# Performance work log

Hardware: AMD Instinct MI355X
Metric: run time of the kernel (lower is better)

Reference implementation:

```python
import jax, jax.numpy as jnp
import numpy as np

N = 50000        # nodes
E = 640000       # edges
D = 128          # emb_dim
L = 3            # num_layer
EDGE_DIM = 8
BN_EPS = 1e-5


def setup_inputs() -> dict:
    key = jax.random.key(0)
    ks = jax.random.split(key, 6)
    return dict(
        x=jax.random.normal(ks[0], (N, D), jnp.float32),
        edge_index=jax.random.randint(ks[1], (2, E), 0, N),
        edge_attr=jax.random.normal(ks[2], (E, EDGE_DIM), jnp.float32),
        eps=jnp.zeros((L,), jnp.float32),
        We=jax.random.normal(ks[3], (L, EDGE_DIM, D), jnp.float32) * 0.1,
        be=jnp.zeros((L, D), jnp.float32),
        W1=jax.random.normal(ks[4], (L, D, 2 * D), jnp.float32) * (1.0 / np.sqrt(D)),
        b1=jnp.zeros((L, 2 * D), jnp.float32),
        g1=jnp.ones((L, 2 * D), jnp.float32),
        bt1=jnp.zeros((L, 2 * D), jnp.float32),
        W2=jax.random.normal(ks[5], (L, 2 * D, D), jnp.float32) * (1.0 / np.sqrt(2 * D)),
        b2=jnp.zeros((L, D), jnp.float32),
        gbn=jnp.ones((L, D), jnp.float32),
        bbn=jnp.zeros((L, D), jnp.float32),
    )


def _bn(h, g, b):
    # BatchNorm1d, training-mode statistics over the node/batch axis
    mu = h.mean(axis=0)
    var = h.var(axis=0)
    return (h - mu) * jax.lax.rsqrt(var + BN_EPS) * g + b


def reference(x, edge_index, edge_attr, eps, We, be, W1, b1, g1, bt1, W2, b2, gbn, bbn):
    src, dst = edge_index[0], edge_index[1]
    h = x
    for l in range(L):
        # GINConv: edge-encoded messages, relu, scatter-add aggregation
        ee = edge_attr @ We[l] + be[l]                      # [E, D]
        msg = jax.nn.relu(h[src] + ee)                      # [E, D]
        agg = jax.ops.segment_sum(msg, dst, num_segments=N)  # [N, D]
        z = (1.0 + eps[l]) * h + agg
        # GIN MLP: Linear -> BN -> ReLU -> Linear
        z = jax.nn.relu(_bn(z @ W1[l] + b1[l], g1[l], bt1[l]))
        z = z @ W2[l] + b2[l]
        # outer per-layer BatchNorm; ReLU on all but the last layer (dropout = eval identity)
        z = _bn(z, gbn[l], bbn[l])
        if l < L - 1:
            z = jax.nn.relu(z)
        h = z  # residual=False, so no skip add
    return h  # JK == 'last'
```

## Files before the change

### kernel.cpp

```cpp
#include <hip/hip_runtime.h>

#define N_NODES 50000
#define N_EDGES 640000
#define D 128
#define D2 256
#define BN_EPS 1e-5f

typedef unsigned short ushort_t;
typedef unsigned int uint_t;

using bf16x8 = __attribute__((ext_vector_type(8))) short;
using f32x4  = __attribute__((ext_vector_type(4))) float;

__device__ inline ushort_t f2bf(float f) {
    uint_t u = __builtin_bit_cast(uint_t, f);
    u = (u + 0x7fffu + ((u >> 16) & 1u)) >> 16;
    return (ushort_t)u;
}
__device__ inline float bf2f(uint_t bits_lo16) {
    return __builtin_bit_cast(float, bits_lo16 << 16);
}

__global__ __launch_bounds__(256) void hist_kernel(
    const int* __restrict__ dst, int* __restrict__ hist)
{
    const int e = blockIdx.x * 256 + threadIdx.x;
    if (e < N_EDGES) atomicAdd(&hist[dst[e]], 1);
}

__global__ __launch_bounds__(256) void scan1_kernel(
    const int* __restrict__ hist, int* __restrict__ scanA,
    int* __restrict__ bsum)
{
    __shared__ int sm[256];
    const int t = threadIdx.x;
    const int idx = blockIdx.x * 256 + t;
    int val = (idx < N_NODES) ? hist[idx] : 0;
    sm[t] = val;
    __syncthreads();
#pragma unroll
    for (int off = 1; off < 256; off <<= 1) {
        const int add = (t >= off) ? sm[t - off] : 0;
        __syncthreads();
        val += add;
        sm[t] = val;
        __syncthreads();
    }
    scanA[idx] = val;
    if (t == 255) bsum[blockIdx.x] = val;
}

__global__ __launch_bounds__(256) void scan2_kernel(
    const int* __restrict__ bsum, int* __restrict__ bscan, int nb)
{
    __shared__ int sm[256];
    const int t = threadIdx.x;
    int val = (t < nb) ? bsum[t] : 0;
    sm[t] = val;
    __syncthreads();
#pragma unroll
    for (int off = 1; off < 256; off <<= 1) {
        const int add = (t >= off) ? sm[t - off] : 0;
        __syncthreads();
        val += add;
        sm[t] = val;
        __syncthreads();
    }
    bscan[t] = val;
}

__global__ __launch_bounds__(256) void scan3_kernel(
    const int* __restrict__ hist, const int* __restrict__ scanA,
    const int* __restrict__ bscan, int* __restrict__ excl)
{
    const int idx = blockIdx.x * 256 + threadIdx.x;
    if (idx < N_NODES) {
        const int carry = blockIdx.x ? bscan[blockIdx.x - 1] : 0;
        const int incl = scanA[idx] + carry;
        excl[idx] = incl - hist[idx];
        if (idx == N_NODES - 1) excl[N_NODES] = incl;
    }
}

__global__ __launch_bounds__(256) void scatter_kernel(
    const int* __restrict__ src, const int* __restrict__ dst,
    const float* __restrict__ ea, int* __restrict__ cursor,
    int* __restrict__ srcp_s, float* __restrict__ ea_s)
{
    const int e = blockIdx.x * 256 + threadIdx.x;
    if (e < N_EDGES) {
        const int t = dst[e];
        const int p = atomicAdd(&cursor[t], 1);
        srcp_s[p] = src[e];
        *(float4*)&ea_s[(size_t)p * 8]     = *(const float4*)&ea[(size_t)e * 8];
        *(float4*)&ea_s[(size_t)p * 8 + 4] = *(const float4*)&ea[(size_t)e * 8 + 4];
    }
}

__global__ __launch_bounds__(256) void wtrans_kernel(
    const float* __restrict__ in, ushort_t* __restrict__ out, int K, int Nt)
{
    __shared__ float tile[32][33];
    const int l = blockIdx.z;
    in  += (size_t)l * K * Nt;
    out += (size_t)l * K * Nt;
    const int n0 = blockIdx.x * 32, k0 = blockIdx.y * 32;
    const int tx = threadIdx.x & 31, ty = threadIdx.x >> 5;
#pragma unroll
    for (int i = 0; i < 32; i += 8)
        tile[ty + i][tx] = in[(size_t)(k0 + ty + i) * Nt + n0 + tx];
    __syncthreads();
#pragma unroll
    for (int i = 0; i < 32; i += 8)
        out[(size_t)(n0 + ty + i) * K + k0 + tx] = f2bf(tile[tx][ty + i]);
}

__device__ __forceinline__ void msg_accum(
    const float* __restrict__ hv, const float* __restrict__ eav,
    const float (&wv)[8][8], const float* __restrict__ bev,
    float* __restrict__ acc)
{
    float m[8];
#pragma unroll
    for (int j = 0; j < 8; ++j) m[j] = bev[j];
#pragma unroll
    for (int k = 0; k < 8; ++k)
#pragma unroll
        for (int j = 0; j < 8; ++j)
            m[j] = fmaf(eav[k], wv[k][j], m[j]);
#pragma unroll
    for (int j = 0; j < 8; ++j)
        acc[j] += fmaxf(hv[j] + m[j], 0.f);
}

__device__ __forceinline__ void unpack_bn_relu(
    const uint4 v, const float* __restrict__ scv,
    const float* __restrict__ shv, float* __restrict__ hv)
{
    float f[8];
    f[0] = bf2f(v.x & 0xffffu); f[1] = bf2f(v.x >> 16);
    f[2] = bf2f(v.y & 0xffffu); f[3] = bf2f(v.y >> 16);
    f[4] = bf2f(v.z & 0xffffu); f[5] = bf2f(v.z >> 16);
    f[6] = bf2f(v.w & 0xffffu); f[7] = bf2f(v.w >> 16);
#pragma unroll
    for (int j = 0; j < 8; ++j)
        hv[j] = fmaxf(fmaf(f[j], scv[j], shv[j]), 0.f);
}

__device__ __forceinline__ void store_z(
    ushort_t* __restrict__ z, int node, int d0, float epsv,
    const float* __restrict__ hn, const float* __restrict__ acc)
{
    uint_t w[8];
#pragma unroll
    for (int j = 0; j < 8; ++j)
        w[j] = (uint_t)f2bf(fmaf(epsv, hn[j], acc[j]));
    uint4 o;
    o.x = w[0] | (w[1] << 16);
    o.y = w[2] | (w[3] << 16);
    o.z = w[4] | (w[5] << 16);
    o.w = w[6] | (w[7] << 16);
    *(uint4*)&z[(size_t)node * D + d0] = o;
}

__global__ __launch_bounds__(256) void agg_z_f32_kernel(
    const float* __restrict__ h, const int* __restrict__ excl,
    const int* __restrict__ srcp_s, const float* __restrict__ ea_s,
    const float* __restrict__ We_l, const float* __restrict__ be_l,
    const float* __restrict__ eps_l, ushort_t* __restrict__ z)
{
    const int lane = threadIdx.x & 63;
    const int wave = threadIdx.x >> 6;
    const int node = blockIdx.x * 4 + wave;
    const int grp  = lane >> 4;
    const int gl   = lane & 15;
    const int d0   = gl * 8;

    float wv[8][8];
#pragma unroll
    for (int k = 0; k < 8; ++k) {
        *(float4*)&wv[k][0] = *(const float4*)&We_l[k * D + d0];
        *(float4*)&wv[k][4] = *(const float4*)&We_l[k * D + d0 + 4];
    }
    float bev[8];
    *(float4*)&bev[0] = *(const float4*)&be_l[d0];
    *(float4*)&bev[4] = *(const float4*)&be_l[d0 + 4];

    const int p0 = excl[node];
    const int p1 = excl[node + 1];
    const int deg = p1 - p0;
    const int scached = (lane < deg) ? srcp_s[p0 + lane] : 0;
    const int nmain = deg < 64 ? deg : 64;

    float acc[8] = {0.f, 0.f, 0.f, 0.f, 0.f, 0.f, 0.f, 0.f};

    if (deg > 0) {
        const int niter = (nmain + 7) >> 3;
        int qA = grp, qB = grp + 4;
        float eA[8], hA[8], eB[8], hB[8];
        for (int it = 0; it < niter - 1; ++it) {
            const int sA = __shfl(scached, qA);
            const int sB = __shfl(scached, qB);
            *(float4*)&eA[0] = *(const float4*)&ea_s[(size_t)(p0 + qA) * 8];
            *(float4*)&eA[4] = *(const float4*)&ea_s[(size_t)(p0 + qA) * 8 + 4];
            *(float4*)&hA[0] = *(const float4*)&h[(size_t)sA * D + d0];
            *(float4*)&hA[4] = *(const float4*)&h[(size_t)sA * D + d0 + 4];
            *(float4*)&eB[0] = *(const float4*)&ea_s[(size_t)(p0 + qB) * 8];
            *(float4*)&eB[4] = *(const float4*)&ea_s[(size_t)(p0 + qB) * 8 + 4];
            *(float4*)&hB[0] = *(const float4*)&h[(size_t)sB * D + d0];
            *(float4*)&hB[4] = *(const float4*)&h[(size_t)sB * D + d0 + 4];
            msg_accum(hA, eA, wv, bev, acc);
            msg_accum(hB, eB, wv, bev, acc);
            qA += 8; qB += 8;
        }
        const int cA = (qA < nmain) ? qA : 0;
        const int cB = (qB < nmain) ? qB : 0;
        const int sA = __shfl(scached, cA);
        const int sB = __shfl(scached, cB);
        if (qA < nmain) {
            *(float4*)&eA[0] = *(const float4*)&ea_s[(size_t)(p0 + qA) * 8];
            *(float4*)&eA[4] = *(const float4*)&ea_s[(size_t)(p0 + qA) * 8 + 4];
            *(float4*)&hA[0] = *(const float4*)&h[(size_t)sA * D + d0];
            *(float4*)&hA[4] = *(const float4*)&h[(size_t)sA * D + d0 + 4];
            msg_accum(hA, eA, wv, bev, acc);
        }
        if (qB < nmain) {
            *(float4*)&eB[0] = *(const float4*)&ea_s[(size_t)(p0 + qB) * 8];
            *(float4*)&eB[4] = *(const float4*)&ea_s[(size_t)(p0 + qB) * 8 + 4];
            *(float4*)&hB[0] = *(const float4*)&h[(size_t)sB * D + d0];
            *(float4*)&hB[4] = *(const float4*)&h[(size_t)sB * D + d0 + 4];
            msg_accum(hB, eB, wv, bev, acc);
        }
    }
    for (int p = p0 + 64 + grp; p < p1; p += 4) {
        const int s = srcp_s[p];
        float eT[8], hT[8];
        *(float4*)&eT[0] = *(const float4*)&ea_s[(size_t)p * 8];
        *(float4*)&eT[4] = *(const float4*)&ea_s[(size_t)p * 8 + 4];
        *(float4*)&hT[0] = *(const float4*)&h[(size_t)s * D + d0];
        *(float4*)&hT[4] = *(const float4*)&h[(size_t)s * D + d0 + 4];
        msg_accum(hT, eT, wv, bev, acc);
    }

#pragma unroll
    for (int j = 0; j < 8; ++j) {
        acc[j] += __shfl_xor(acc[j], 16);
        acc[j] += __shfl_xor(acc[j], 32);
    }

    if (grp == 0) {
        float hn[8];
        *(float4*)&hn[0] = *(const float4*)&h[(size_t)node * D + d0];
        *(float4*)&hn[4] = *(const float4*)&h[(size_t)node * D + d0 + 4];
        store_z(z, node, d0, 1.0f + eps_l[0], hn, acc);
    }
}

__global__ __launch_bounds__(256) void agg_z_bf16_kernel(
    const ushort_t* __restrict__ t2, const float* __restrict__ sc2,
    const float* __restrict__ sh2, const int* __restrict__ excl,
    const int* __restrict__ srcp_s, const float* __restrict__ ea_s,
    const float* __restrict__ We_l, const float* __restrict__ be_l,
    const float* __restrict__ eps_l, ushort_t* __restrict__ z)
{
    const int lane = threadIdx.x & 63;
    const int wave = threadIdx.x >> 6;
    const int node = blockIdx.x * 4 + wave;
    const int grp  = lane >> 4;
    const int gl   = lane & 15;
    const int d0   = gl * 8;

    float wv[8][8];
#pragma unroll
    for (int k = 0; k < 8; ++k) {
        *(float4*)&wv[k][0] = *(const float4*)&We_l[k * D + d0];
        *(float4*)&wv[k][4] = *(const float4*)&We_l[k * D + d0 + 4];
    }
    float bev[8], scv[8], shv[8];
    *(float4*)&bev[0] = *(const float4*)&be_l[d0];
    *(float4*)&bev[4] = *(const float4*)&be_l[d0 + 4];
    *(float4*)&scv[0] = *(const float4*)&sc2[d0];
    *(float4*)&scv[4] = *(const float4*)&sc2[d0 + 4];
    *(float4*)&shv[0] = *(const float4*)&sh2[d0];
    *(float4*)&shv[4] = *(const float4*)&sh2[d0 + 4];

    const int p0 = excl[node];
    const int p1 = excl[node + 1];
    const int deg = p1 - p0;
    const int scached = (lane < deg) ? srcp_s[p0 + lane] : 0;
    const int nmain = deg < 64 ? deg : 64;

    float acc[8] = {0.f, 0.f, 0.f, 0.f, 0.f, 0.f, 0.f, 0.f};

    if (deg > 0) {
        const int niter = (nmain + 7) >> 3;
        int qA = grp, qB = grp + 4;
        float eA[8], eB[8], hA[8], hB[8];
        uint4 vA, vB;
        for (int it = 0; it < niter - 1; ++it) {
            const int sA = __shfl(scached, qA);
            const int sB = __shfl(scached, qB);
            *(float4*)&eA[0] = *(const float4*)&ea_s[(size_t)(p0 + qA) * 8];
            *(float4*)&eA[4] = *(const float4*)&ea_s[(size_t)(p0 + qA) * 8 + 4];
            vA = *(const uint4*)&t2[(size_t)sA * D + d0];
            *(float4*)&eB[0] = *(const float4*)&ea_s[(size_t)(p0 + qB) * 8];
            *(float4*)&eB[4] = *(const float4*)&ea_s[(size_t)(p0 + qB) * 8 + 4];
            vB = *(const uint4*)&t2[(size_t)sB * D + d0];
            unpack_bn_relu(vA, scv, shv, hA);
            msg_accum(hA, eA, wv, bev, acc);
            unpack_bn_relu(vB, scv, shv, hB);
            msg_accum(hB, eB, wv, bev, acc);
            qA += 8; qB += 8;
        }
        const int cA = (qA < nmain) ? qA : 0;
        const int cB = (qB < nmain) ? qB : 0;
        const int sA = __shfl(scached, cA);
        const int sB = __shfl(scached, cB);
        if (qA < nmain) {
            *(float4*)&eA[0] = *(const float4*)&ea_s[(size_t)(p0 + qA) * 8];
            *(float4*)&eA[4] = *(const float4*)&ea_s[(size_t)(p0 + qA) * 8 + 4];
            vA = *(const uint4*)&t2[(size_t)sA * D + d0];
            unpack_bn_relu(vA, scv, shv, hA);
            msg_accum(hA, eA, wv, bev, acc);
        }
        if (qB < nmain) {
            *(float4*)&eB[0] = *(const float4*)&ea_s[(size_t)(p0 + qB) * 8];
            *(float4*)&eB[4] = *(const float4*)&ea_s[(size_t)(p0 + qB) * 8 + 4];
            vB = *(const uint4*)&t2[(size_t)sB * D + d0];
            unpack_bn_relu(vB, scv, shv, hB);
            msg_accum(hB, eB, wv, bev, acc);
        }
    }
    for (int p = p0 + 64 + grp; p < p1; p += 4) {
        const int s = srcp_s[p];
        float eT[8], hT[8];
        *(float4*)&eT[0] = *(const float4*)&ea_s[(size_t)p * 8];
        *(float4*)&eT[4] = *(const float4*)&ea_s[(size_t)p * 8 + 4];
        const uint4 vT = *(const uint4*)&t2[(size_t)s * D + d0];
        unpack_bn_relu(vT, scv, shv, hT);
        msg_accum(hT, eT, wv, bev, acc);
    }

#pragma unroll
    for (int j = 0; j < 8; ++j) {
        acc[j] += __shfl_xor(acc[j], 16);
        acc[j] += __shfl_xor(acc[j], 32);
    }

    if (grp == 0) {
        const uint4 vN = *(const uint4*)&t2[(size_t)node * D + d0];
        float hn[8];
        unpack_bn_relu(vN, scv, shv, hn);
        store_z(z, node, d0, 1.0f + eps_l[0], hn, acc);
    }
}

template<int KTILES>
__global__ __launch_bounds__(256) void gemm_bf16_kernel(
    const ushort_t* __restrict__ A, const ushort_t* __restrict__ Bt,
    const float* __restrict__ bias, ushort_t* __restrict__ out,
    float* __restrict__ gsum, float* __restrict__ gsq)
{
    __shared__ ushort_t As[128][136];
    __shared__ ushort_t Bs[128][136];
    __shared__ float ls_sum[128], ls_sq[128];
    const int tid = threadIdx.x;
    const int M0 = blockIdx.x * 128;
    const int N0 = blockIdx.y * 128;
    const int Ntot = gridDim.y * 128;
    const int K = KTILES * 128;
    if (tid < 128) { ls_sum[tid] = 0.f; ls_sq[tid] = 0.f; }
    const int lane = tid & 63, w = tid >> 6;
    const int wm = w >> 1, wn = w & 1;
    const int lr = lane & 15;
    const int lk = (lane >> 4) * 8;
    f32x4 acc[4][4] = {};

    for (int kt = 0; kt < KTILES; ++kt) {
        if (kt) __syncthreads();
#pragma unroll
        for (int p = 0; p < 8; ++p) {
            const int idx = p * 256 + tid;
            const int row = idx >> 4, ch = (idx & 15) * 8;
            uint4 v = make_uint4(0, 0, 0, 0);
            const int gr = M0 + row;
            if (gr < N_NODES)
                v = *(const uint4*)&A[(size_t)gr * K + kt * 128 + ch];
            *(uint4*)&As[row][ch] = v;
        }
#pragma unroll
        for (int p = 0; p < 8; ++p) {
            const int idx = p * 256 + tid;
            const int row = idx >> 4, ch = (idx & 15) * 8;
            *(uint4*)&Bs[row][ch] =
                *(const uint4*)&Bt[(size_t)(N0 + row) * K + kt * 128 + ch];
        }
        __syncthreads();
#pragma unroll
        for (int ks = 0; ks < 4; ++ks) {
            const int kof = ks * 32 + lk;
            bf16x8 af[4], bfr[4];
#pragma unroll
            for (int mi = 0; mi < 4; ++mi)
                af[mi] = *(const bf16x8*)&As[wm * 64 + mi * 16 + lr][kof];
#pragma unroll
            for (int ni = 0; ni < 4; ++ni)
                bfr[ni] = *(const bf16x8*)&Bs[wn * 64 + ni * 16 + lr][kof];
#pragma unroll
            for (int mi = 0; mi < 4; ++mi)
#pragma unroll
                for (int ni = 0; ni < 4; ++ni)
                    acc[mi][ni] = __builtin_amdgcn_mfma_f32_16x16x32_bf16(
                        af[mi], bfr[ni], acc[mi][ni], 0, 0, 0);
        }
    }
    __syncthreads();

#pragma unroll
    for (int ni = 0; ni < 4; ++ni) {
        const int cl = wn * 64 + ni * 16 + lr;
        const float bv = bias[N0 + cl];
        float ps = 0.f, pq = 0.f;
#pragma unroll
        for (int mi = 0; mi < 4; ++mi) {
            const int rbase = M0 + wm * 64 + mi * 16 + (lane >> 4) * 4;
#pragma unroll
            for (int r = 0; r < 4; ++r) {
                const int row = rbase + r;
                if (row < N_NODES) {
                    const float v = acc[mi][ni][r] + bv;
                    out[(size_t)row * Ntot + N0 + cl] = f2bf(v);
                    ps += v;
                    pq += v * v;
                }
            }
        }
        atomicAdd(&ls_sum[cl], ps);
        atomicAdd(&ls_sq[cl], pq);
    }
    __syncthreads();
    if (tid < 128) {
        unsafeAtomicAdd(&gsum[N0 + tid], ls_sum[tid]);
        unsafeAtomicAdd(&gsq[N0 + tid], ls_sq[tid]);
    }
}

__global__ __launch_bounds__(256) void gemm2_bn_kernel(
    const ushort_t* __restrict__ A, const float* __restrict__ sc1,
    const float* __restrict__ sh1, const ushort_t* __restrict__ Bt,
    const float* __restrict__ bias, ushort_t* __restrict__ out,
    float* __restrict__ gsum, float* __restrict__ gsq)
{
    __shared__ ushort_t As[128][136];
    __shared__ ushort_t Bs[128][136];
    __shared__ float ls_sum[128], ls_sq[128];
    const int tid = threadIdx.x;
    const int M0 = blockIdx.x * 128;
    const int K = 256, Ntot = 128;
    if (tid < 128) { ls_sum[tid] = 0.f; ls_sq[tid] = 0.f; }
    const int lane = tid & 63, w = tid >> 6;
    const int wm = w >> 1, wn = w & 1;
    const int lr = lane & 15;
    const int lk = (lane >> 4) * 8;
    f32x4 acc[4][4] = {};

    for (int kt = 0; kt < 2; ++kt) {
        if (kt) __syncthreads();
#pragma unroll
        for (int p = 0; p < 8; ++p) {
            const int idx = p * 256 + tid;
            const int row = idx >> 4, ch = (idx & 15) * 8;
            const int col = kt * 128 + ch;
            uint4 v = make_uint4(0, 0, 0, 0);
            const int gr = M0 + row;
            if (gr < N_NODES) {
                const uint4 t = *(const uint4*)&A[(size_t)gr * K + col];
                float f[8];
                f[0] = bf2f(t.x & 0xffffu); f[1] = bf2f(t.x >> 16);
                f[2] = bf2f(t.y & 0xffffu); f[3] = bf2f(t.y >> 16);
                f[4] = bf2f(t.z & 0xffffu); f[5] = bf2f(t.z >> 16);
                f[6] = bf2f(t.w & 0xffffu); f[7] = bf2f(t.w >> 16);
                const float4 s0 = *(const float4*)&sc1[col];
                const float4 s1 = *(const float4*)&sc1[col + 4];
                const float4 h0 = *(const float4*)&sh1[col];
                const float4 h1 = *(const float4*)&sh1[col + 4];
                f[0] = fmaxf(fmaf(f[0], s0.x, h0.x), 0.f);
                f[1] = fmaxf(fmaf(f[1], s0.y, h0.y), 0.f);
                f[2] = fmaxf(fmaf(f[2], s0.z, h0.z), 0.f);
                f[3] = fmaxf(fmaf(f[3], s0.w, h0.w), 0.f);
                f[4] = fmaxf(fmaf(f[4], s1.x, h1.x), 0.f);
                f[5] = fmaxf(fmaf(f[5], s1.y, h1.y), 0.f);
                f[6] = fmaxf(fmaf(f[6], s1.z, h1.z), 0.f);
                f[7] = fmaxf(fmaf(f[7], s1.w, h1.w), 0.f);
                v.x = (uint_t)f2bf(f[0]) | ((uint_t)f2bf(f[1]) << 16);
                v.y = (uint_t)f2bf(f[2]) | ((uint_t)f2bf(f[3]) << 16);
                v.z = (uint_t)f2bf(f[4]) | ((uint_t)f2bf(f[5]) << 16);
                v.w = (uint_t)f2bf(f[6]) | ((uint_t)f2bf(f[7]) << 16);
            }
            *(uint4*)&As[row][ch] = v;
        }
#pragma unroll
        for (int p = 0; p < 8; ++p) {
            const int idx = p * 256 + tid;
            const int row = idx >> 4, ch = (idx & 15) * 8;
            *(uint4*)&Bs[row][ch] =
                *(const uint4*)&Bt[(size_t)row * K + kt * 128 + ch];
        }
        __syncthreads();
#pragma unroll
        for (int ks = 0; ks < 4; ++ks) {
            const int kof = ks * 32 + lk;
            bf16x8 af[4], bfr[4];
#pragma unroll
            for (int mi = 0; mi < 4; ++mi)
                af[mi] = *(const bf16x8*)&As[wm * 64 + mi * 16 + lr][kof];
#pragma unroll
            for (int ni = 0; ni < 4; ++ni)
                bfr[ni] = *(const bf16x8*)&Bs[wn * 64 + ni * 16 + lr][kof];
#pragma unroll
            for (int mi = 0; mi < 4; ++mi)
#pragma unroll
                for (int ni = 0; ni < 4; ++ni)
                    acc[mi][ni] = __builtin_amdgcn_mfma_f32_16x16x32_bf16(
                        af[mi], bfr[ni], acc[mi][ni], 0, 0, 0);
        }
    }
    __syncthreads();

#pragma unroll
    for (int ni = 0; ni < 4; ++ni) {
        const int cl = wn * 64 + ni * 16 + lr;
        const float bv = bias[cl];
        float ps = 0.f, pq = 0.f;
#pragma unroll
        for (int mi = 0; mi < 4; ++mi) {
            const int rbase = M0 + wm * 64 + mi * 16 + (lane >> 4) * 4;
#pragma unroll
            for (int r = 0; r < 4; ++r) {
                const int row = rbase + r;
                if (row < N_NODES) {
                    const float v = acc[mi][ni][r] + bv;
                    out[(size_t)row * Ntot + cl] = f2bf(v);
                    ps += v;
                    pq += v * v;
                }
            }
        }
        atomicAdd(&ls_sum[cl], ps);
        atomicAdd(&ls_sq[cl], pq);
    }
    __syncthreads();
    if (tid < 128) {
        unsafeAtomicAdd(&gsum[tid], ls_sum[tid]);
        unsafeAtomicAdd(&gsq[tid], ls_sq[tid]);
    }
}

__global__ void bnparam_kernel(const float* __restrict__ gsum,
                               const float* __restrict__ gsq,
                               const float* __restrict__ g,
                               const float* __restrict__ bt,
                               float* __restrict__ scale,
                               float* __restrict__ shift, int C)
{
    const int c = threadIdx.x;
    if (c < C) {
        const float inv_n = 1.0f / (float)N_NODES;
        const float mu = gsum[c] * inv_n;
        const float var = gsq[c] * inv_n - mu * mu;
        const float s = g[c] * rsqrtf(var + BN_EPS);
        scale[c] = s;
        shift[c] = bt[c] - mu * s;
    }
}

__global__ __launch_bounds__(256) void bnapply2_kernel(
    const ushort_t* __restrict__ t, const float* __restrict__ sc,
    const float* __restrict__ sh, float* __restrict__ outp)
{
    const size_t idx = (size_t)blockIdx.x * 256 + threadIdx.x;
    const int c = (int)(idx & 15) * 8;
    const uint4 v = ((const uint4*)t)[idx];
    const float4 s0 = *(const float4*)&sc[c];
    const float4 s1 = *(const float4*)&sc[c + 4];
    const float4 h0 = *(const float4*)&sh[c];
    const float4 h1 = *(const float4*)&sh[c + 4];
    float4 r0, r1;
    r0.x = fmaf(bf2f(v.x & 0xffffu), s0.x, h0.x);
    r0.y = fmaf(bf2f(v.x >> 16),     s0.y, h0.y);
    r0.z = fmaf(bf2f(v.y & 0xffffu), s0.z, h0.z);
    r0.w = fmaf(bf2f(v.y >> 16),     s0.w, h0.w);
    r1.x = fmaf(bf2f(v.z & 0xffffu), s1.x, h1.x);
    r1.y = fmaf(bf2f(v.z >> 16),     s1.y, h1.y);
    r1.z = fmaf(bf2f(v.w & 0xffffu), s1.z, h1.z);
    r1.w = fmaf(bf2f(v.w >> 16),     s1.w, h1.w);
    *(float4*)&outp[idx * 8]     = r0;
    *(float4*)&outp[idx * 8 + 4] = r1;
}

extern "C" void kernel_launch(void* const* d_in, const int* in_sizes, int n_in,
                              void* d_out, int out_size, void* d_ws, size_t ws_size,
                              hipStream_t stream)
{
    const float* x         = (const float*)d_in[0];
    const int*   edge_index= (const int*)d_in[1];
    const float* edge_attr = (const float*)d_in[2];
    const float* eps       = (const float*)d_in[3];
    const float* We        = (const float*)d_in[4];
    const float* be        = (const float*)d_in[5];
    const float* W1        = (const float*)d_in[6];
    const float* b1        = (const float*)d_in[7];
    const float* g1        = (const float*)d_in[8];
    const float* bt1       = (const float*)d_in[9];
    const float* W2        = (const float*)d_in[10];
    const float* b2        = (const float*)d_in[11];
    const float* gbn       = (const float*)d_in[12];
    const float* bbn       = (const float*)d_in[13];
    float* out = (float*)d_out;

    float* ws = (float*)d_ws;
    const size_t ND = (size_t)N_NODES * D;
    float* EAS  = ws;
    float* ZB   = EAS + (size_t)N_EDGES * 8;
    float* T2B  = ZB + ND / 2;
    float* T1B  = T2B + ND / 2;
    float* STATS = T1B + ND;
    float* gsum1 = STATS;
    float* gsq1  = gsum1 + 3 * 256;
    float* gsum2 = gsq1 + 3 * 256;
    float* gsq2  = gsum2 + 3 * 128;
    float* scale1 = gsq2 + 3 * 128;
    float* shift1 = scale1 + 256;
    float* sc2buf = shift1 + 256;
    float* sh2buf = sc2buf + 3 * 128;

    ushort_t* zbuf  = (ushort_t*)ZB;
    ushort_t* t2buf = (ushort_t*)T2B;
    ushort_t* t1buf = (ushort_t*)T1B;

    int* hist   = (int*)T1B;
    int* scanA  = hist + N_NODES;
    int* bsum   = scanA + 50176;
    int* bscan  = bsum + 256;
    int* cursor = bscan + 256;

    int* srcp_s = (int*)d_out;
    int* excl   = srcp_s + N_EDGES;
    ushort_t* W1t = (ushort_t*)((int*)d_out + 690008);
    ushort_t* W2t = W1t + 3 * D2 * D;

    const int* srcp = edge_index;
    const int* dstp = edge_index + N_EDGES;

    hipMemsetAsync(STATS, 0, 2304 * sizeof(float), stream);
    hipMemsetAsync(hist, 0, N_NODES * sizeof(int), stream);

    const int EB = (N_EDGES + 255) / 256;
    const int NB = (N_NODES + 255) / 256;
    hist_kernel<<<EB, 256, 0, stream>>>(dstp, hist);
    scan1_kernel<<<NB, 256, 0, stream>>>(hist, scanA, bsum);
    scan2_kernel<<<1, 256, 0, stream>>>(bsum, bscan, NB);
    scan3_kernel<<<NB, 256, 0, stream>>>(hist, scanA, bscan, excl);
    hipMemcpyAsync(cursor, excl, N_NODES * sizeof(int),
                   hipMemcpyDeviceToDevice, stream);
    scatter_kernel<<<EB, 256, 0, stream>>>(srcp, dstp, edge_attr,
                                           cursor, srcp_s, EAS);

    wtrans_kernel<<<dim3(8, 4, 3), 256, 0, stream>>>(W1, W1t, D, D2);
    wtrans_kernel<<<dim3(4, 8, 3), 256, 0, stream>>>(W2, W2t, D2, D);

    for (int l = 0; l < 3; ++l) {
        if (l == 0) {
            agg_z_f32_kernel<<<N_NODES / 4, 256, 0, stream>>>(
                x, excl, srcp_s, EAS,
                We + (size_t)l * 8 * D, be + (size_t)l * D, eps + l, zbuf);
        } else {
            agg_z_bf16_kernel<<<N_NODES / 4, 256, 0, stream>>>(
                t2buf, sc2buf + (l - 1) * 128, sh2buf + (l - 1) * 128,
                excl, srcp_s, EAS,
                We + (size_t)l * 8 * D, be + (size_t)l * D, eps + l, zbuf);
        }

        dim3 grid1((N_NODES + 127) / 128, 2);
        gemm_bf16_kernel<1><<<grid1, 256, 0, stream>>>(
            zbuf, W1t + (size_t)l * D2 * D, b1 + (size_t)l * D2,
            t1buf, gsum1 + l * 256, gsq1 + l * 256);

        bnparam_kernel<<<1, 256, 0, stream>>>(
            gsum1 + l * 256, gsq1 + l * 256,
            g1 + (size_t)l * D2, bt1 + (size_t)l * D2, scale1, shift1, D2);

        dim3 grid2((N_NODES + 127) / 128, 1);
        gemm2_bn_kernel<<<grid2, 256, 0, stream>>>(
            t1buf, scale1, shift1,
            W2t + (size_t)l * D * D2, b2 + (size_t)l * D, t2buf,
            gsum2 + l * 128, gsq2 + l * 128);

        bnparam_kernel<<<1, 256, 0, stream>>>(
            gsum2 + l * 128, gsq2 + l * 128,
            gbn + (size_t)l * D, bbn + (size_t)l * D,
            sc2buf + l * 128, sh2buf + l * 128, D);
    }

    bnapply2_kernel<<<(N_NODES * D / 8) / 256, 256, 0, stream>>>(
        t2buf, sc2buf + 2 * 128, sh2buf + 2 * 128, out);
}
```

Measured before the change: 656.5 us.

## Replace LDS-tiled GEMMs with register-resident weight fragments and direct global A loads

```diff
diff --git a/kernel.cpp b/kernel.cpp
--- a/kernel.cpp
+++ b/kernel.cpp
@@ -355,81 +355,62 @@
     }
 }
 
-template<int KTILES>
-__global__ __launch_bounds__(256) void gemm_bf16_kernel(
+__global__ __launch_bounds__(256) void gemm1_reg_kernel(
     const ushort_t* __restrict__ A, const ushort_t* __restrict__ Bt,
     const float* __restrict__ bias, ushort_t* __restrict__ out,
     float* __restrict__ gsum, float* __restrict__ gsq)
 {
-    __shared__ ushort_t As[128][136];
-    __shared__ ushort_t Bs[128][136];
-    __shared__ float ls_sum[128], ls_sq[128];
+    __shared__ float ls_sum[D2], ls_sq[D2];
     const int tid = threadIdx.x;
-    const int M0 = blockIdx.x * 128;
-    const int N0 = blockIdx.y * 128;
-    const int Ntot = gridDim.y * 128;
-    const int K = KTILES * 128;
-    if (tid < 128) { ls_sum[tid] = 0.f; ls_sq[tid] = 0.f; }
-    const int lane = tid & 63, w = tid >> 6;
-    const int wm = w >> 1, wn = w & 1;
+    const int lane = tid & 63, wn = tid >> 6;
     const int lr = lane & 15;
     const int lk = (lane >> 4) * 8;
+    const int M0 = blockIdx.x * 64;
+    ls_sum[tid] = 0.f; ls_sq[tid] = 0.f;
+    __syncthreads();
+
+    bf16x8 bfr[4][4];
+#pragma unroll
+    for (int ni = 0; ni < 4; ++ni)
+#pragma unroll
+        for (int ks = 0; ks < 4; ++ks)
+            bfr[ni][ks] = *(const bf16x8*)
+                &Bt[(size_t)(wn * 64 + ni * 16 + lr) * D + ks * 32 + lk];
+
+    const bf16x8 zfrag = {};
     f32x4 acc[4][4] = {};
-
-    for (int kt = 0; kt < KTILES; ++kt) {
-        if (kt) __syncthreads();
-#pragma unroll
-        for (int p = 0; p < 8; ++p) {
-            const int idx = p * 256 + tid;
-            const int row = idx >> 4, ch = (idx & 15) * 8;
-            uint4 v = make_uint4(0, 0, 0, 0);
-            const int gr = M0 + row;
-            if (gr < N_NODES)
-                v = *(const uint4*)&A[(size_t)gr * K + kt * 128 + ch];
-            *(uint4*)&As[row][ch] = v;
-        }
-#pragma unroll
-        for (int p = 0; p < 8; ++p) {
-            const int idx = p * 256 + tid;
-            const int row = idx >> 4, ch = (idx & 15) * 8;
-            *(uint4*)&Bs[row][ch] =
-                *(const uint4*)&Bt[(size_t)(N0 + row) * K + kt * 128 + ch];
-        }
-        __syncthreads();
-#pragma unroll
-        for (int ks = 0; ks < 4; ++ks) {
-            const int kof = ks * 32 + lk;
-            bf16x8 af[4], bfr[4];
-#pragma unroll
-            for (int mi = 0; mi < 4; ++mi)
-                af[mi] = *(const bf16x8*)&As[wm * 64 + mi * 16 + lr][kof];
+#pragma unroll
+    for (int ks = 0; ks < 4; ++ks) {
+        bf16x8 af[4];
+#pragma unroll
+        for (int mi = 0; mi < 4; ++mi) {
+            const int row = M0 + mi * 16 + lr;
+            af[mi] = (row < N_NODES)
+                ? *(const bf16x8*)&A[(size_t)row * D + ks * 32 + lk]
+                : zfrag;
+        }
+#pragma unroll
+        for (int mi = 0; mi < 4; ++mi)
 #pragma unroll
             for (int ni = 0; ni < 4; ++ni)
-                bfr[ni] = *(const bf16x8*)&Bs[wn * 64 + ni * 16 + lr][kof];
-#pragma unroll
-            for (int mi = 0; mi < 4; ++mi)
-#pragma unroll
-                for (int ni = 0; ni < 4; ++ni)
-                    acc[mi][ni] = __builtin_amdgcn_mfma_f32_16x16x32_bf16(
-                        af[mi], bfr[ni], acc[mi][ni], 0, 0, 0);
-        }
-    }
-    __syncthreads();
+                acc[mi][ni] = __builtin_amdgcn_mfma_f32_16x16x32_bf16(
+                    af[mi], bfr[ni][ks], acc[mi][ni], 0, 0, 0);
+    }
 
 #pragma unroll
     for (int ni = 0; ni < 4; ++ni) {
         const int cl = wn * 64 + ni * 16 + lr;
-        const float bv = bias[N0 + cl];
+        const float bv = bias[cl];
         float ps = 0.f, pq = 0.f;
 #pragma unroll
         for (int mi = 0; mi < 4; ++mi) {
-            const int rbase = M0 + wm * 64 + mi * 16 + (lane >> 4) * 4;
+            const int rbase = M0 + mi * 16 + (lane >> 4) * 4;
 #pragma unroll
             for (int r = 0; r < 4; ++r) {
                 const int row = rbase + r;
                 if (row < N_NODES) {
                     const float v = acc[mi][ni][r] + bv;
-                    out[(size_t)row * Ntot + N0 + cl] = f2bf(v);
+                    out[(size_t)row * D2 + cl] = f2bf(v);
                     ps += v;
                     pq += v * v;
                 }
@@ -439,108 +420,86 @@
         atomicAdd(&ls_sq[cl], pq);
     }
     __syncthreads();
-    if (tid < 128) {
-        unsafeAtomicAdd(&gsum[N0 + tid], ls_sum[tid]);
-        unsafeAtomicAdd(&gsq[N0 + tid], ls_sq[tid]);
-    }
-}
-
-__global__ __launch_bounds__(256) void gemm2_bn_kernel(
+    unsafeAtomicAdd(&gsum[tid], ls_sum[tid]);
+    unsafeAtomicAdd(&gsq[tid], ls_sq[tid]);
+}
+
+__global__ __launch_bounds__(256) void gemm2_reg_kernel(
     const ushort_t* __restrict__ A, const float* __restrict__ sc1,
     const float* __restrict__ sh1, const ushort_t* __restrict__ Bt,
     const float* __restrict__ bias, ushort_t* __restrict__ out,
     float* __restrict__ gsum, float* __restrict__ gsq)
 {
-    __shared__ ushort_t As[128][136];
-    __shared__ ushort_t Bs[128][136];
-    __shared__ float ls_sum[128], ls_sq[128];
+    __shared__ float ls_sum[D], ls_sq[D];
     const int tid = threadIdx.x;
-    const int M0 = blockIdx.x * 128;
-    const int K = 256, Ntot = 128;
-    if (tid < 128) { ls_sum[tid] = 0.f; ls_sq[tid] = 0.f; }
-    const int lane = tid & 63, w = tid >> 6;
-    const int wm = w >> 1, wn = w & 1;
+    const int lane = tid & 63, wn = tid >> 6;
     const int lr = lane & 15;
     const int lk = (lane >> 4) * 8;
-    f32x4 acc[4][4] = {};
-
-    for (int kt = 0; kt < 2; ++kt) {
-        if (kt) __syncthreads();
-#pragma unroll
-        for (int p = 0; p < 8; ++p) {
-            const int idx = p * 256 + tid;
-            const int row = idx >> 4, ch = (idx & 15) * 8;
-            const int col = kt * 128 + ch;
-            uint4 v = make_uint4(0, 0, 0, 0);
-            const int gr = M0 + row;
-            if (gr < N_NODES) {
-                const uint4 t = *(const uint4*)&A[(size_t)gr * K + col];
+    const int M0 = blockIdx.x * 64;
+    if (tid < D) { ls_sum[tid] = 0.f; ls_sq[tid] = 0.f; }
+    __syncthreads();
+
+    bf16x8 bfr[2][8];
+#pragma unroll
+    for (int ni = 0; ni < 2; ++ni)
+#pragma unroll
+        for (int ks = 0; ks < 8; ++ks)
+            bfr[ni][ks] = *(const bf16x8*)
+                &Bt[(size_t)(wn * 32 + ni * 16 + lr) * D2 + ks * 32 + lk];
+
+    f32x4 acc[4][2] = {};
+#pragma unroll
+    for (int ks = 0; ks < 8; ++ks) {
+        const int kc = ks * 32 + lk;
+        float scv[8], shv[8];
+        *(float4*)&scv[0] = *(const float4*)&sc1[kc];
+        *(float4*)&scv[4] = *(const float4*)&sc1[kc + 4];
+        *(float4*)&shv[0] = *(const float4*)&sh1[kc];
+        *(float4*)&shv[4] = *(const float4*)&sh1[kc + 4];
+        bf16x8 af[4];
+#pragma unroll
+        for (int mi = 0; mi < 4; ++mi) {
+            const int row = M0 + mi * 16 + lr;
+            uint4 pk = make_uint4(0, 0, 0, 0);
+            if (row < N_NODES) {
+                const uint4 t = *(const uint4*)&A[(size_t)row * D2 + kc];
                 float f[8];
                 f[0] = bf2f(t.x & 0xffffu); f[1] = bf2f(t.x >> 16);
                 f[2] = bf2f(t.y & 0xffffu); f[3] = bf2f(t.y >> 16);
                 f[4] = bf2f(t.z & 0xffffu); f[5] = bf2f(t.z >> 16);
                 f[6] = bf2f(t.w & 0xffffu); f[7] = bf2f(t.w >> 16);
-                const float4 s0 = *(const float4*)&sc1[col];
-                const float4 s1 = *(const float4*)&sc1[col + 4];
-                const float4 h0 = *(const float4*)&sh1[col];
-                const float4 h1 = *(const float4*)&sh1[col + 4];
-                f[0] = fmaxf(fmaf(f[0], s0.x, h0.x), 0.f);
-                f[1] = fmaxf(fmaf(f[1], s0.y, h0.y), 0.f);
-                f[2] = fmaxf(fmaf(f[2], s0.z, h0.z), 0.f);
-                f[3] = fmaxf(fmaf(f[3], s0.w, h0.w), 0.f);
-                f[4] = fmaxf(fmaf(f[4], s1.x, h1.x), 0.f);
-                f[5] = fmaxf(fmaf(f[5], s1.y, h1.y), 0.f);
-                f[6] = fmaxf(fmaf(f[6], s1.z, h1.z), 0.f);
-                f[7] = fmaxf(fmaf(f[7], s1.w, h1.w), 0.f);
-                v.x = (uint_t)f2bf(f[0]) | ((uint_t)f2bf(f[1]) << 16);
-                v.y = (uint_t)f2bf(f[2]) | ((uint_t)f2bf(f[3]) << 16);
-                v.z = (uint_t)f2bf(f[4]) | ((uint_t)f2bf(f[5]) << 16);
-                v.w = (uint_t)f2bf(f[6]) | ((uint_t)f2bf(f[7]) << 16);
+#pragma unroll
+                for (int j = 0; j < 8; ++j)
+                    f[j] = fmaxf(fmaf(f[j], scv[j], shv[j]), 0.f);
+                pk.x = (uint_t)f2bf(f[0]) | ((uint_t)f2bf(f[1]) << 16);
+                pk.y = (uint_t)f2bf(f[2]) | ((uint_t)f2bf(f[3]) << 16);
+                pk.z = (uint_t)f2bf(f[4]) | ((uint_t)f2bf(f[5]) << 16);
+                pk.w = (uint_t)f2bf(f[6]) | ((uint_t)f2bf(f[7]) << 16);
             }
-            *(uint4*)&As[row][ch] = v;
-        }
-#pragma unroll
-        for (int p = 0; p < 8; ++p) {
-            const int idx = p * 256 + tid;
-            const int row = idx >> 4, ch = (idx & 15) * 8;
-            *(uint4*)&Bs[row][ch] =
-                *(const uint4*)&Bt[(size_t)row * K + kt * 128 + ch];
-        }
-        __syncthreads();
-#pragma unroll
-        for (int ks = 0; ks < 4; ++ks) {
-            const int kof = ks * 32 + lk;
-            bf16x8 af[4], bfr[4];
-#pragma unroll
-            for (int mi = 0; mi < 4; ++mi)
-                af[mi] = *(const bf16x8*)&As[wm * 64 + mi * 16 + lr][kof];
-#pragma unroll
-            for (int ni = 0; ni < 4; ++ni)
-                bfr[ni] = *(const bf16x8*)&Bs[wn * 64 + ni * 16 + lr][kof];
-#pragma unroll
-            for (int mi = 0; mi < 4; ++mi)
-#pragma unroll
-                for (int ni = 0; ni < 4; ++ni)
-                    acc[mi][ni] = __builtin_amdgcn_mfma_f32_16x16x32_bf16(
-                        af[mi], bfr[ni], acc[mi][ni], 0, 0, 0);
-        }
-    }
-    __syncthreads();
-
-#pragma unroll
-    for (int ni = 0; ni < 4; ++ni) {
-        const int cl = wn * 64 + ni * 16 + lr;
+            af[mi] = __builtin_bit_cast(bf16x8, pk);
+        }
+#pragma unroll
+        for (int mi = 0; mi < 4; ++mi)
+#pragma unroll
+            for (int ni = 0; ni < 2; ++ni)
+                acc[mi][ni] = __builtin_amdgcn_mfma_f32_16x16x32_bf16(
+                    af[mi], bfr[ni][ks], acc[mi][ni], 0, 0, 0);
+    }
+
+#pragma unroll
+    for (int ni = 0; ni < 2; ++ni) {
+        const int cl = wn * 32 + ni * 16 + lr;
         const float bv = bias[cl];
         float ps = 0.f, pq = 0.f;
 #pragma unroll
         for (int mi = 0; mi < 4; ++mi) {
-            const int rbase = M0 + wm * 64 + mi * 16 + (lane >> 4) * 4;
+            const int rbase = M0 + mi * 16 + (lane >> 4) * 4;
 #pragma unroll
             for (int r = 0; r < 4; ++r) {
                 const int row = rbase + r;
                 if (row < N_NODES) {
                     const float v = acc[mi][ni][r] + bv;
-                    out[(size_t)row * Ntot + cl] = f2bf(v);
+                    out[(size_t)row * D + cl] = f2bf(v);
                     ps += v;
                     pq += v * v;
                 }
@@ -550,7 +509,7 @@
         atomicAdd(&ls_sq[cl], pq);
     }
     __syncthreads();
-    if (tid < 128) {
+    if (tid < D) {
         unsafeAtomicAdd(&gsum[tid], ls_sum[tid]);
         unsafeAtomicAdd(&gsq[tid], ls_sq[tid]);
     }
@@ -669,6 +628,8 @@
     wtrans_kernel<<<dim3(8, 4, 3), 256, 0, stream>>>(W1, W1t, D, D2);
     wtrans_kernel<<<dim3(4, 8, 3), 256, 0, stream>>>(W2, W2t, D2, D);
 
+    const int MG = (N_NODES + 63) / 64;
+
     for (int l = 0; l < 3; ++l) {
         if (l == 0) {
             agg_z_f32_kernel<<<N_NODES / 4, 256, 0, stream>>>(
@@ -681,8 +642,7 @@
                 We + (size_t)l * 8 * D, be + (size_t)l * D, eps + l, zbuf);
         }
 
-        dim3 grid1((N_NODES + 127) / 128, 2);
-        gemm_bf16_kernel<1><<<grid1, 256, 0, stream>>>(
+        gemm1_reg_kernel<<<MG, 256, 0, stream>>>(
             zbuf, W1t + (size_t)l * D2 * D, b1 + (size_t)l * D2,
             t1buf, gsum1 + l * 256, gsq1 + l * 256);
 
@@ -690,8 +650,7 @@
             gsum1 + l * 256, gsq1 + l * 256,
             g1 + (size_t)l * D2, bt1 + (size_t)l * D2, scale1, shift1, D2);
 
-        dim3 grid2((N_NODES + 127) / 128, 1);
-        gemm2_bn_kernel<<<grid2, 256, 0, stream>>>(
+        gemm2_reg_kernel<<<MG, 256, 0, stream>>>(
             t1buf, scale1, shift1,
             W2t + (size_t)l * D * D2, b2 + (size_t)l * D, t2buf,
             gsum2 + l * 128, gsq2 + l * 128);
```

Result: slower. 749.7 us (+14.2%).
